# Kernel optimization log

Measured on AMD Instinct MI355X. Metric: run time of the kernel, lower is better.

Reference implementation:

```python
import jax, jax.numpy as jnp
import numpy as np

GRID_SIZE = 5
SPLINE_ORDER = 3
N_COEF = GRID_SIZE + SPLINE_ORDER  # 8 spline basis coefficients per input feature


def _grid(dtype):
    # grid_range = [-1, 1]; h = 2/grid_size; knots from -spline_order*h-1 to ...
    h = 2.0 / GRID_SIZE
    return (jnp.arange(-SPLINE_ORDER, GRID_SIZE + SPLINE_ORDER + 1, dtype=dtype) * h - 1.0)


def b_splines(x):
    # x: (N, in_features) -> (N, in_features, N_COEF) via Cox-de Boor recursion
    grid = _grid(x.dtype)  # (grid_size + 2*spline_order + 1,) shared across features
    xg = x[:, :, None]
    bases = ((xg >= grid[:-1]) & (xg < grid[1:])).astype(x.dtype)
    for k in range(1, SPLINE_ORDER + 1):
        left = (xg - grid[: -(k + 1)]) / (grid[k:-1] - grid[: -(k + 1)]) * bases[..., :-1]
        right = (grid[k + 1:] - xg) / (grid[k + 1:] - grid[1:-k]) * bases[..., 1:]
        bases = left + right
    return bases


def kan_linear(x, base_w, spline_w, scaler):
    # base path: silu(x) @ base_w.T ; spline path: bases contracted with scaled spline weight
    base_out = jnp.dot(jax.nn.silu(x), base_w.T)
    bases = b_splines(x)  # (N, in, C)
    sw = spline_w * scaler[:, :, None]  # (out, in, C)
    spline_out = jnp.einsum('nic,oic->no', bases, sw)
    return base_out + spline_out


def setup_inputs() -> dict:
    key = jax.random.key(0)
    ks = jax.random.split(key, 8)
    b, s, d_model, d_ff = 2, 2048, 1024, 4096
    x = jax.random.normal(ks[0], (b, s, d_model), dtype=jnp.float32)
    def mk(kw, kk, out_f, in_f):
        base_w = jax.random.normal(kw, (out_f, in_f), dtype=jnp.float32) * (1.0 / np.sqrt(in_f))
        spline_w = jax.random.normal(kk, (out_f, in_f, N_COEF), dtype=jnp.float32) * (0.1 / np.sqrt(in_f))
        scaler = jnp.ones((out_f, in_f), dtype=jnp.float32)
        return base_w, spline_w, scaler
    base_w1, spline_w1, scaler1 = mk(ks[1], ks[2], d_ff, d_model)
    base_w2, spline_w2, scaler2 = mk(ks[3], ks[4], d_model, d_ff)
    return {"x": x, "base_w1": base_w1, "spline_w1": spline_w1, "scaler1": scaler1,
            "base_w2": base_w2, "spline_w2": spline_w2, "scaler2": scaler2}


def reference(x, base_w1, spline_w1, scaler1, base_w2, spline_w2, scaler2):
    b, s, d = x.shape
    h = x.reshape(-1, d)
    h = kan_linear(h, base_w1, spline_w1, scaler1)
    h = kan_linear(h, base_w2, spline_w2, scaler2)
    return h.reshape(b, s, d)
```

## Files before the change

kernel.cpp:

```cpp
#include <hip/hip_runtime.h>


typedef unsigned short u16;
typedef __bf16 bf16x8 __attribute__((ext_vector_type(8)));
typedef float f32x4 __attribute__((ext_vector_type(4)));
typedef u16 u16x8 __attribute__((ext_vector_type(8)));

#define D_MODEL 1024
#define D_FF    4096
#define NTOK    4096
#define K1      9216
#define K2      36864
#define KCHUNK  9216

__device__ __forceinline__ u16 f2bf(float v) {
    union { float f; unsigned u; } a; a.f = v;
    unsigned r = a.u + 0x7FFFu + ((a.u >> 16) & 1u);
    return (u16)(r >> 16);
}

__device__ __forceinline__ float silu_f(float x) {
    return x / (1.f + __expf(-x));
}

__device__ __forceinline__ void llds16(const u16* g, u16* l) {
    __builtin_amdgcn_global_load_lds(
        (__attribute__((address_space(1))) void*)(u16*)g,
        (__attribute__((address_space(3))) void*)l,
        16, 0, 0);
}

__global__ __launch_bounds__(256) void build_w(
    const float* __restrict__ bw, const float* __restrict__ sw,
    const float* __restrict__ sc, u16* __restrict__ dst,
    int IN, int shift)
{
    const int idx = blockIdx.x * 256 + threadIdx.x;
    const int o = idx >> shift;
    const int i = idx & (IN - 1);
    const int rowLen = IN * 9;
    const float scv = sc[idx];
    const float* sp = sw + (size_t)idx * 8;
    f32x4 s0 = *(const f32x4*)sp;
    f32x4 s1 = *(const f32x4*)(sp + 4);
    u16x8 p;
#pragma unroll
    for (int t = 0; t < 4; ++t) {
        p[t]     = f2bf(s0[t] * scv);
        p[t + 4] = f2bf(s1[t] * scv);
    }
    dst[(size_t)o * rowLen + i] = f2bf(bw[idx]);
    *(u16x8*)(dst + (size_t)o * rowLen + IN + (size_t)i * 8) = p;
}

__global__ __launch_bounds__(128) void build_act(
    const float* __restrict__ src, int srcCols,
    u16* __restrict__ dst, int col0)
{
    const int g = blockIdx.x * 128 + threadIdx.x;
    const int n = blockIdx.y;
    const int base = col0 + g * 8;
    u16x8 p;
    if (base < srcCols) {
        const float* sp = src + (size_t)n * srcCols + base;
        f32x4 v0 = *(const f32x4*)sp;
        f32x4 v1 = *(const f32x4*)(sp + 4);
#pragma unroll
        for (int t = 0; t < 4; ++t) {
            p[t]     = f2bf(silu_f(v0[t]));
            p[t + 4] = f2bf(silu_f(v1[t]));
        }
    } else {
        const int i = (base - srcCols) >> 3;
        const float xv = src[(size_t)n * srcCols + i];
        const float t = (xv + 2.2f) * 2.5f;
        const bool inr = (t >= 0.f) && (t < 11.f);
        const float jf = floorf(t);
        const int j = (int)jf;
        const float f = t - jf;
        const float f2 = f * f, f3 = f2 * f;
        const float s6 = 1.f / 6.f;
        const float w3 = f3 * s6;
        const float w2 = (1.f + 3.f*f + 3.f*f2 - 3.f*f3) * s6;
        const float w1 = (4.f - 6.f*f2 + 3.f*f3) * s6;
        float w0 = 1.f - f; w0 = w0 * w0 * w0 * s6;
#pragma unroll
        for (int c = 0; c < 8; ++c) {
            float v = 0.f;
            v = (j == c)     ? w3 : v;
            v = (j == c + 1) ? w2 : v;
            v = (j == c + 2) ? w1 : v;
            v = (j == c + 3) ? w0 : v;
            v = inr ? v : 0.f;
            p[c] = f2bf(v);
        }
    }
    *(u16x8*)(dst + (size_t)n * 9216 + (size_t)g * 8) = p;
}

template <int WMODE>
__global__ __launch_bounds__(512, 2) void gemm256(
    const u16* __restrict__ A, int lda,
    const u16* __restrict__ B, int ldb,
    float* __restrict__ C, int ldc,
    int nk, size_t zstride)
{
    __shared__ __attribute__((aligned(16))) u16 sm[2][2][2][256][32];

    const int tid  = threadIdx.x;
    const int lane = tid & 63;
    const int wave = tid >> 6;
    const int wr = wave >> 2;
    const int wc = wave & 3;

    const int gx = gridDim.x, gy = gridDim.y, gz = gridDim.z;
    int flat = (blockIdx.z * gy + blockIdx.y) * gx + blockIdx.x;
    const int nwg = gx * gy * gz;
    const int cpx = nwg >> 3;
    flat = (flat & 7) * cpx + (flat >> 3);
    const int bx = flat % gx;
    const int by = (flat / gx) % gy;
    const int bz = flat / (gx * gy);

    const int m0 = by * 256;
    const int n0 = bx * 256;
    const int k0 = bz * nk * 64;

    const int sRow  = tid >> 2;
    const int swcol = ((tid & 3) ^ ((tid >> 3) & 3)) * 8;
    const u16* Ag0 = A + (size_t)(m0 + sRow)       * lda + k0 + swcol;
    const u16* Ag1 = A + (size_t)(m0 + 128 + sRow) * lda + k0 + swcol;
    const u16* Bg0 = B + (size_t)(n0 + sRow)       * ldb + k0 + swcol;
    const u16* Bg1 = B + (size_t)(n0 + 128 + sRow) * ldb + k0 + swcol;

    const int fRow = lane & 15;
    const int ucol = (((lane >> 4) ^ ((lane >> 1) & 3))) * 8;

    const f32x4 zero = {0.f, 0.f, 0.f, 0.f};
    f32x4 acc[8][4];
#pragma unroll
    for (int a = 0; a < 8; ++a)
#pragma unroll
        for (int b = 0; b < 4; ++b) acc[a][b] = zero;

#pragma unroll
    for (int p = 0; p < 4; ++p) {
        const size_t koff = (size_t)(p >> 1) * 32;
        u16* lb = &sm[0][p & 1][p >> 1][0][0] + wave * 512;
        if ((p & 1) == 0) { llds16(Ag0 + koff, lb); llds16(Ag1 + koff, lb + 4096); }
        else              { llds16(Bg0 + koff, lb); llds16(Bg1 + koff, lb + 4096); }
    }
    asm volatile("s_waitcnt vmcnt(4)" ::: "memory");
    __builtin_amdgcn_s_barrier();
    __builtin_amdgcn_sched_barrier(0);

    bf16x8 bb[4];
    for (int kt = 0; kt < nk; ++kt) {
        const int b = kt & 1;
        const int ktn = (kt + 1 < nk) ? kt + 1 : 0;
#pragma unroll
        for (int p = 0; p < 4; ++p) {
            const int ks = p >> 1, mh = p & 1;
            bf16x8 af[4];
#pragma unroll
            for (int j = 0; j < 4; ++j)
                af[j] = *(const bf16x8*)
                    &sm[b][0][ks][wr * 128 + mh * 64 + j * 16 + fRow][ucol];
            if (mh == 0) {
#pragma unroll
                for (int nf = 0; nf < 4; ++nf)
                    bb[nf] = *(const bf16x8*)
                        &sm[b][1][ks][wc * 64 + nf * 16 + fRow][ucol];
            }
            {
                const size_t koff = (size_t)ktn * 64 + (size_t)(p >> 1) * 32;
                u16* lb = &sm[b ^ 1][p & 1][p >> 1][0][0] + wave * 512;
                if ((p & 1) == 0) { llds16(Ag0 + koff, lb); llds16(Ag1 + koff, lb + 4096); }
                else              { llds16(Bg0 + koff, lb); llds16(Bg1 + koff, lb + 4096); }
            }
            asm volatile("s_waitcnt lgkmcnt(0)" ::: "memory");
            __builtin_amdgcn_sched_barrier(0);
            __builtin_amdgcn_s_setprio(1);
#pragma unroll
            for (int j = 0; j < 4; ++j)
#pragma unroll
                for (int nf = 0; nf < 4; ++nf)
                    acc[mh * 4 + j][nf] = __builtin_amdgcn_mfma_f32_16x16x32_bf16(
                        af[j], bb[nf], acc[mh * 4 + j][nf], 0, 0, 0);
            __builtin_amdgcn_s_setprio(0);
            __builtin_amdgcn_sched_barrier(0);
            if (p == 1 || p == 3)
                asm volatile("s_waitcnt vmcnt(4)" ::: "memory");
            __builtin_amdgcn_s_barrier();
            __builtin_amdgcn_sched_barrier(0);
        }
    }
    asm volatile("s_waitcnt vmcnt(0)" ::: "memory");

    float* Cz = C + (size_t)bz * zstride;
    const int cRow = m0 + wr * 128 + (lane >> 4) * 4;
    const int cCol = n0 + wc * 64 + (lane & 15);
#pragma unroll
    for (int af = 0; af < 8; ++af)
#pragma unroll
        for (int nf = 0; nf < 4; ++nf)
#pragma unroll
            for (int j = 0; j < 4; ++j) {
                const size_t off = (size_t)(cRow + af * 16 + j) * ldc
                                 + (cCol + nf * 16);
                if (WMODE == 1)      atomicAdd(&Cz[off], acc[af][nf][j]);
                else if (WMODE == 2) Cz[off] += acc[af][nf][j];
                else                 Cz[off] = acc[af][nf][j];
            }
}

__global__ __launch_bounds__(256) void reduce4(
    const float* __restrict__ z, float* __restrict__ out, int n4, int zstride4)
{
    const int i = blockIdx.x * 256 + threadIdx.x;
    if (i >= n4) return;
    const f32x4* p = (const f32x4*)z;
    f32x4 v = p[i];
    v += p[i + zstride4];
    v += p[i + 2 * zstride4];
    v += p[i + 3 * zstride4];
    *(f32x4*)(out + (size_t)i * 4) = v;
}

extern "C" void kernel_launch(void* const* d_in, const int* in_sizes, int n_in,
                              void* d_out, int out_size, void* d_ws, size_t ws_size,
                              hipStream_t stream) {
    const float* x   = (const float*)d_in[0];
    const float* bw1 = (const float*)d_in[1];
    const float* sw1 = (const float*)d_in[2];
    const float* sc1 = (const float*)d_in[3];
    const float* bw2 = (const float*)d_in[4];
    const float* sw2 = (const float*)d_in[5];
    const float* sc2 = (const float*)d_in[6];
    float* out = (float*)d_out;

    char* ws = (char*)d_ws;
    u16*   regionA = (u16*)ws;
    u16*   regionB = (u16*)(ws + 75497472);
    float* hbuf    = (float*)(ws + 150994944);
    float* zbuf    = (float*)(ws + 218103808);
    const bool useZ = ws_size >= 285212672ull;
    const size_t ZS = (size_t)NTOK * D_MODEL;

    if (!useZ)
        hipMemsetAsync(d_out, 0, ZS * sizeof(float), stream);

    build_w<<<16384, 256, 0, stream>>>(bw1, sw1, sc1, regionA, D_MODEL, 10);
    build_act<<<dim3(9, NTOK), 128, 0, stream>>>(x, D_MODEL, regionB, 0);
    gemm256<0><<<dim3(16, 16, 1), 512, 0, stream>>>(
        regionB, K1, regionA, K1, hbuf, D_FF, 144, 0);

    build_w<<<16384, 256, 0, stream>>>(bw2, sw2, sc2, regionB, D_FF, 12);
    for (int ck = 0; ck < 4; ++ck) {
        build_act<<<dim3(9, NTOK), 128, 0, stream>>>(hbuf, D_FF, regionA, ck * KCHUNK);
        if (useZ) {
            if (ck == 0)
                gemm256<0><<<dim3(4, 16, 4), 512, 0, stream>>>(
                    regionA, KCHUNK, regionB + (size_t)ck * KCHUNK, K2,
                    zbuf, D_MODEL, 36, ZS);
            else
                gemm256<2><<<dim3(4, 16, 4), 512, 0, stream>>>(
                    regionA, KCHUNK, regionB + (size_t)ck * KCHUNK, K2,
                    zbuf, D_MODEL, 36, ZS);
        } else {
            gemm256<1><<<dim3(4, 16, 4), 512, 0, stream>>>(
                regionA, KCHUNK, regionB + (size_t)ck * KCHUNK, K2,
                out, D_MODEL, 36, ZS);
        }
    }
    if (useZ)
        reduce4<<<(int)(ZS / 4 / 256), 256, 0, stream>>>(zbuf, out, (int)(ZS / 4), (int)(ZS / 4));
}
```

Before: 1.050 ms.

## Fuse SiLU into GEMM1 epilogue and compute B-spline bases inside GEMM2 loader

The first GEMM's epilogue now also writes a bf16 SiLU copy of its output. The second layer no longer materializes the full 36864-wide activation matrix in four chunks. Instead, the base part runs as a plain GEMM on the SiLU buffer, and a new gemm_bas kernel reads fp32 hidden values, computes the 8 B-spline bases in registers and stores them straight to LDS before the MFMA loop. This removes the four build_act passes and their large intermediate writes and reads, at the cost of extra ALU work and a different synchronisation pattern inside the GEMM pipeline.

```diff
diff --git a/kernel.cpp b/kernel.cpp
--- a/kernel.cpp
+++ b/kernel.cpp
@@ -21,6 +21,32 @@
 
 __device__ __forceinline__ float silu_f(float x) {
     return x / (1.f + __expf(-x));
+}
+
+__device__ __forceinline__ u16x8 bases8(float xv) {
+    const float t = (xv + 2.2f) * 2.5f;
+    const bool inr = (t >= 0.f) && (t < 11.f);
+    const float jf = floorf(t);
+    const int j = (int)jf;
+    const float f = t - jf;
+    const float f2 = f * f, f3 = f2 * f;
+    const float s6 = 1.f / 6.f;
+    const float w3 = f3 * s6;
+    const float w2 = (1.f + 3.f*f + 3.f*f2 - 3.f*f3) * s6;
+    const float w1 = (4.f - 6.f*f2 + 3.f*f3) * s6;
+    float w0 = 1.f - f; w0 = w0 * w0 * w0 * s6;
+    u16x8 p;
+#pragma unroll
+    for (int c = 0; c < 8; ++c) {
+        float v = 0.f;
+        v = (j == c)     ? w3 : v;
+        v = (j == c + 1) ? w2 : v;
+        v = (j == c + 2) ? w1 : v;
+        v = (j == c + 3) ? w0 : v;
+        v = inr ? v : 0.f;
+        p[c] = f2bf(v);
+    }
+    return p;
 }
 
 __device__ __forceinline__ void llds16(const u16* g, u16* l) {
@@ -55,7 +81,7 @@
 
 __global__ __launch_bounds__(128) void build_act(
     const float* __restrict__ src, int srcCols,
-    u16* __restrict__ dst, int col0)
+    u16* __restrict__ dst, int col0, int ldDst)
 {
     const int g = blockIdx.x * 128 + threadIdx.x;
     const int n = blockIdx.y;
@@ -72,30 +98,9 @@
         }
     } else {
         const int i = (base - srcCols) >> 3;
-        const float xv = src[(size_t)n * srcCols + i];
-        const float t = (xv + 2.2f) * 2.5f;
-        const bool inr = (t >= 0.f) && (t < 11.f);
-        const float jf = floorf(t);
-        const int j = (int)jf;
-        const float f = t - jf;
-        const float f2 = f * f, f3 = f2 * f;
-        const float s6 = 1.f / 6.f;
-        const float w3 = f3 * s6;
-        const float w2 = (1.f + 3.f*f + 3.f*f2 - 3.f*f3) * s6;
-        const float w1 = (4.f - 6.f*f2 + 3.f*f3) * s6;
-        float w0 = 1.f - f; w0 = w0 * w0 * w0 * s6;
-#pragma unroll
-        for (int c = 0; c < 8; ++c) {
-            float v = 0.f;
-            v = (j == c)     ? w3 : v;
-            v = (j == c + 1) ? w2 : v;
-            v = (j == c + 2) ? w1 : v;
-            v = (j == c + 3) ? w0 : v;
-            v = inr ? v : 0.f;
-            p[c] = f2bf(v);
-        }
-    }
-    *(u16x8*)(dst + (size_t)n * 9216 + (size_t)g * 8) = p;
+        p = bases8(src[(size_t)n * srcCols + i]);
+    }
+    *(u16x8*)(dst + (size_t)n * ldDst + (size_t)g * 8) = p;
 }
 
 template <int WMODE>
@@ -103,7 +108,7 @@
     const u16* __restrict__ A, int lda,
     const u16* __restrict__ B, int ldb,
     float* __restrict__ C, int ldc,
-    int nk, size_t zstride)
+    int nk, size_t zstride, u16* __restrict__ actOut)
 {
     __shared__ __attribute__((aligned(16))) u16 sm[2][2][2][256][32];
 
@@ -197,6 +202,164 @@
     }
     asm volatile("s_waitcnt vmcnt(0)" ::: "memory");
 
+    const int cRow = m0 + wr * 128 + (lane >> 4) * 4;
+    const int cCol = n0 + wc * 64 + (lane & 15);
+    if (WMODE == 4) {
+#pragma unroll
+        for (int af = 0; af < 8; ++af)
+#pragma unroll
+            for (int nf = 0; nf < 4; ++nf)
+#pragma unroll
+                for (int j = 0; j < 4; ++j) {
+                    const int row = cRow + af * 16 + j;
+                    const int col = cCol + nf * 16;
+                    const float v = acc[af][nf][j];
+                    C[(size_t)row * ldc + col] = v;
+                    actOut[(size_t)row * 4096 + col] = f2bf(silu_f(v));
+                }
+    } else {
+        float* Cz = C + (size_t)bz * zstride;
+#pragma unroll
+        for (int af = 0; af < 8; ++af)
+#pragma unroll
+            for (int nf = 0; nf < 4; ++nf)
+#pragma unroll
+                for (int j = 0; j < 4; ++j) {
+                    const size_t off = (size_t)(cRow + af * 16 + j) * ldc
+                                     + (cCol + nf * 16);
+                    if (WMODE == 1)      atomicAdd(&Cz[off], acc[af][nf][j]);
+                    else if (WMODE == 2) Cz[off] += acc[af][nf][j];
+                    else                 Cz[off] = acc[af][nf][j];
+                }
+    }
+}
+
+__global__ __launch_bounds__(512, 2) void gemm_bas(
+    const float* __restrict__ h,
+    const u16* __restrict__ B, int ldb,
+    float* __restrict__ C, int ldc,
+    int nk, size_t zstride)
+{
+    __shared__ __attribute__((aligned(16))) u16 sm[2][2][2][256][32];
+
+    const int tid  = threadIdx.x;
+    const int lane = tid & 63;
+    const int wave = tid >> 6;
+    const int wr = wave >> 2;
+    const int wc = wave & 3;
+
+    const int gx = gridDim.x, gy = gridDim.y, gz = gridDim.z;
+    int flat = (blockIdx.z * gy + blockIdx.y) * gx + blockIdx.x;
+    const int nwg = gx * gy * gz;
+    const int cpx = nwg >> 3;
+    flat = (flat & 7) * cpx + (flat >> 3);
+    const int bx = flat % gx;
+    const int by = (flat / gx) % gy;
+    const int bz = flat / (gx * gy);
+
+    const int m0 = by * 256;
+    const int n0 = bx * 256;
+    const int kb0 = bz * nk * 64;
+
+    const int sRow  = tid >> 2;
+    const int swcol = ((tid & 3) ^ ((tid >> 3) & 3)) * 8;
+    const u16* Bg0 = B + (size_t)(n0 + sRow)       * ldb + kb0 + swcol;
+    const u16* Bg1 = B + (size_t)(n0 + 128 + sRow) * ldb + kb0 + swcol;
+
+    const int hr = tid >> 1;
+    const int hh = tid & 1;
+    const float* Hg = h + (size_t)(m0 + hr) * 4096 + (kb0 >> 3) + hh * 4;
+    const int wu = (hr >> 1) & 3;
+    u16* dwA[2] = { &sm[0][0][hh][hr][0], &sm[1][0][hh][hr][0] };
+
+    const int fRow = lane & 15;
+    const int ucol = (((lane >> 4) ^ ((lane >> 1) & 3))) * 8;
+
+    const f32x4 zero = {0.f, 0.f, 0.f, 0.f};
+    f32x4 acc[8][4];
+#pragma unroll
+    for (int a = 0; a < 8; ++a)
+#pragma unroll
+        for (int b = 0; b < 4; ++b) acc[a][b] = zero;
+
+    f32x4 hv = *(const f32x4*)Hg;
+    { u16* lb = &sm[0][1][0][0][0] + wave * 512;
+      llds16(Bg0, lb); llds16(Bg1, lb + 4096); }
+    { u16* lb = &sm[0][1][1][0][0] + wave * 512;
+      llds16(Bg0 + 32, lb); llds16(Bg1 + 32, lb + 4096); }
+    asm volatile("s_waitcnt vmcnt(4)" ::: "memory");
+    __builtin_amdgcn_sched_barrier(0);
+#pragma unroll
+    for (int i = 0; i < 4; ++i) {
+        u16x8 bs = bases8(hv[i]);
+        *(u16x8*)(dwA[0] + (size_t)((i ^ wu) * 8)) = bs;
+    }
+    asm volatile("s_waitcnt vmcnt(0) lgkmcnt(0)" ::: "memory");
+    __builtin_amdgcn_s_barrier();
+    __builtin_amdgcn_sched_barrier(0);
+
+    bf16x8 bb[4];
+    for (int kt = 0; kt < nk; ++kt) {
+        const int b = kt & 1;
+        const int ktn = (kt + 1 < nk) ? kt + 1 : 0;
+        u16* dwN = dwA[b ^ 1];
+#pragma unroll
+        for (int p = 0; p < 4; ++p) {
+            const int ks = p >> 1, mh = p & 1;
+            bf16x8 af[4];
+#pragma unroll
+            for (int j = 0; j < 4; ++j)
+                af[j] = *(const bf16x8*)
+                    &sm[b][0][ks][wr * 128 + mh * 64 + j * 16 + fRow][ucol];
+            if (mh == 0) {
+#pragma unroll
+                for (int nf = 0; nf < 4; ++nf)
+                    bb[nf] = *(const bf16x8*)
+                        &sm[b][1][ks][wc * 64 + nf * 16 + fRow][ucol];
+            }
+            if (p == 0)
+                hv = *(const f32x4*)(Hg + (size_t)ktn * 8);
+            if (p == 1) {
+                u16* lb = &sm[b ^ 1][1][0][0][0] + wave * 512;
+                llds16(Bg0 + (size_t)ktn * 64, lb);
+                llds16(Bg1 + (size_t)ktn * 64, lb + 4096);
+            }
+            if (p == 2) {
+                asm volatile("s_waitcnt vmcnt(2)" ::: "memory");
+                __builtin_amdgcn_sched_barrier(0);
+#pragma unroll
+                for (int i = 0; i < 4; ++i) {
+                    u16x8 bs = bases8(hv[i]);
+                    *(u16x8*)(dwN + (size_t)((i ^ wu) * 8)) = bs;
+                }
+            }
+            if (p == 3) {
+                u16* lb = &sm[b ^ 1][1][1][0][0] + wave * 512;
+                llds16(Bg0 + (size_t)ktn * 64 + 32, lb);
+                llds16(Bg1 + (size_t)ktn * 64 + 32, lb + 4096);
+            }
+            __builtin_amdgcn_s_barrier();
+            asm volatile("s_waitcnt lgkmcnt(0)" ::: "memory");
+            __builtin_amdgcn_sched_barrier(0);
+            __builtin_amdgcn_s_setprio(1);
+#pragma unroll
+            for (int j = 0; j < 4; ++j)
+#pragma unroll
+                for (int nf = 0; nf < 4; ++nf)
+                    acc[mh * 4 + j][nf] = __builtin_amdgcn_mfma_f32_16x16x32_bf16(
+                        af[j], bb[nf], acc[mh * 4 + j][nf], 0, 0, 0);
+            __builtin_amdgcn_s_setprio(0);
+            __builtin_amdgcn_sched_barrier(0);
+            if (p == 1)
+                asm volatile("s_waitcnt vmcnt(3)" ::: "memory");
+            if (p == 3)
+                asm volatile("s_waitcnt vmcnt(2)" ::: "memory");
+            __builtin_amdgcn_s_barrier();
+            __builtin_amdgcn_sched_barrier(0);
+        }
+    }
+    asm volatile("s_waitcnt vmcnt(0)" ::: "memory");
+
     float* Cz = C + (size_t)bz * zstride;
     const int cRow = m0 + wr * 128 + (lane >> 4) * 4;
     const int cCol = n0 + wc * 64 + (lane & 15);
@@ -208,9 +371,7 @@
             for (int j = 0; j < 4; ++j) {
                 const size_t off = (size_t)(cRow + af * 16 + j) * ldc
                                  + (cCol + nf * 16);
-                if (WMODE == 1)      atomicAdd(&Cz[off], acc[af][nf][j]);
-                else if (WMODE == 2) Cz[off] += acc[af][nf][j];
-                else                 Cz[off] = acc[af][nf][j];
+                Cz[off] += acc[af][nf][j];
             }
 }
 
@@ -240,39 +401,46 @@
     float* out = (float*)d_out;
 
     char* ws = (char*)d_ws;
+    const size_t ZS = (size_t)NTOK * D_MODEL;
+
+    if (ws_size >= 251658240ull) {
+        u16*   r0   = (u16*)ws;
+        u16*   r1   = (u16*)(ws + 75497472);
+        float* zbuf = (float*)(ws + 75497472);
+        float* hbuf = (float*)(ws + 150994944);
+        u16*   silu = (u16*)(ws + 218103808);
+
+        build_w<<<16384, 256, 0, stream>>>(bw1, sw1, sc1, r1, D_MODEL, 10);
+        build_act<<<dim3(9, NTOK), 128, 0, stream>>>(x, D_MODEL, r0, 0, K1);
+        gemm256<4><<<dim3(16, 16, 1), 512, 0, stream>>>(
+            r0, K1, r1, K1, hbuf, D_FF, 144, 0, silu);
+
+        build_w<<<16384, 256, 0, stream>>>(bw2, sw2, sc2, r0, D_FF, 12);
+        gemm256<0><<<dim3(4, 16, 4), 512, 0, stream>>>(
+            silu, D_FF, r0, K2, zbuf, D_MODEL, 16, ZS, nullptr);
+        gemm_bas<<<dim3(4, 16, 4), 512, 0, stream>>>(
+            hbuf, r0 + D_FF, K2, zbuf, D_MODEL, 128, ZS);
+        reduce4<<<(int)(ZS / 4 / 256), 256, 0, stream>>>(
+            zbuf, out, (int)(ZS / 4), (int)(ZS / 4));
+        return;
+    }
+
     u16*   regionA = (u16*)ws;
     u16*   regionB = (u16*)(ws + 75497472);
     float* hbuf    = (float*)(ws + 150994944);
-    float* zbuf    = (float*)(ws + 218103808);
-    const bool useZ = ws_size >= 285212672ull;
-    const size_t ZS = (size_t)NTOK * D_MODEL;
-
-    if (!useZ)
-        hipMemsetAsync(d_out, 0, ZS * sizeof(float), stream);
+
+    hipMemsetAsync(d_out, 0, ZS * sizeof(float), stream);
 
     build_w<<<16384, 256, 0, stream>>>(bw1, sw1, sc1, regionA, D_MODEL, 10);
-    build_act<<<dim3(9, NTOK), 128, 0, stream>>>(x, D_MODEL, regionB, 0);
+    build_act<<<dim3(9, NTOK), 128, 0, stream>>>(x, D_MODEL, regionB, 0, K1);
     gemm256<0><<<dim3(16, 16, 1), 512, 0, stream>>>(
-        regionB, K1, regionA, K1, hbuf, D_FF, 144, 0);
+        regionB, K1, regionA, K1, hbuf, D_FF, 144, 0, nullptr);
 
     build_w<<<16384, 256, 0, stream>>>(bw2, sw2, sc2, regionB, D_FF, 12);
     for (int ck = 0; ck < 4; ++ck) {
-        build_act<<<dim3(9, NTOK), 128, 0, stream>>>(hbuf, D_FF, regionA, ck * KCHUNK);
-        if (useZ) {
-            if (ck == 0)
-                gemm256<0><<<dim3(4, 16, 4), 512, 0, stream>>>(
-                    regionA, KCHUNK, regionB + (size_t)ck * KCHUNK, K2,
-                    zbuf, D_MODEL, 36, ZS);
-            else
-                gemm256<2><<<dim3(4, 16, 4), 512, 0, stream>>>(
-                    regionA, KCHUNK, regionB + (size_t)ck * KCHUNK, K2,
-                    zbuf, D_MODEL, 36, ZS);
-        } else {
-            gemm256<1><<<dim3(4, 16, 4), 512, 0, stream>>>(
-                regionA, KCHUNK, regionB + (size_t)ck * KCHUNK, K2,
-                out, D_MODEL, 36, ZS);
-        }
-    }
-    if (useZ)
-        reduce4<<<(int)(ZS / 4 / 256), 256, 0, stream>>>(zbuf, out, (int)(ZS / 4), (int)(ZS / 4));
-}
+        build_act<<<dim3(9, NTOK), 128, 0, stream>>>(hbuf, D_FF, regionA, ck * KCHUNK, K1);
+        gemm256<1><<<dim3(4, 16, 4), 512, 0, stream>>>(
+            regionA, KCHUNK, regionB + (size_t)ck * KCHUNK, K2,
+            out, D_MODEL, 36, ZS, nullptr);
+    }
+}
```

Measured after the change: 1.090 ms. +3.8%, slower.
